# Kernel tuning notes

Hardware: AMD Instinct MI355X
Metric: run time of the kernel (lower is better)

## Reference

```python
import jax, jax.numpy as jnp
import numpy as np

N_NODES = 100000
N_EDGES = 1600000
IN_CH = 128
HID = 128
BN_EPS = 1e-5


def setup_inputs() -> dict:
    key = jax.random.key(0)
    ks = jax.random.split(key, 8)
    s = 1.0 / np.sqrt(HID)
    return {
        "x": jax.random.normal(ks[0], (N_NODES, IN_CH), dtype=jnp.float32),
        "edge_index": jax.random.randint(ks[1], (2, N_EDGES), 0, N_NODES, dtype=jnp.int64),
        "w1_0": jax.random.normal(ks[2], (IN_CH, HID), dtype=jnp.float32) * s,
        "b1_0": jnp.zeros((HID,), dtype=jnp.float32),
        "w2_0": jax.random.normal(ks[3], (HID, HID), dtype=jnp.float32) * s,
        "b2_0": jnp.zeros((HID,), dtype=jnp.float32),
        "gamma_0": jnp.ones((HID,), dtype=jnp.float32),
        "beta_0": jnp.zeros((HID,), dtype=jnp.float32),
        "w1_1": jax.random.normal(ks[4], (HID, HID), dtype=jnp.float32) * s,
        "b1_1": jnp.zeros((HID,), dtype=jnp.float32),
        "w2_1": jax.random.normal(ks[5], (HID, HID), dtype=jnp.float32) * s,
        "b2_1": jnp.zeros((HID,), dtype=jnp.float32),
        "gamma_1": jnp.ones((HID,), dtype=jnp.float32),
        "beta_1": jnp.zeros((HID,), dtype=jnp.float32),
    }


def _gin_layer(x, src, dst, w1, b1, w2, b2, gamma, beta):
    n = x.shape[0]
    # neighbor sum aggregation: scatter-add of source features into destinations
    agg = jax.ops.segment_sum(x[src], dst, num_segments=n)
    h = x + agg  # GINConv with eps = 0: (1 + eps) * x + sum_j x_j
    h = jax.nn.relu(h @ w1 + b1) @ w2 + b2  # 2-layer MLP
    # BatchNorm1d (training mode): batch mean, biased variance
    mean = jnp.mean(h, axis=0)
    var = jnp.mean(jnp.square(h - mean), axis=0)
    h = (h - mean) * jax.lax.rsqrt(var + BN_EPS) * gamma + beta
    return jax.nn.relu(h)


def reference(x, edge_index, w1_0, b1_0, w2_0, b2_0, gamma_0, beta_0,
              w1_1, b1_1, w2_1, b2_1, gamma_1, beta_1):
    src, dst = edge_index[0], edge_index[1]
    h = _gin_layer(x, src, dst, w1_0, b1_0, w2_0, b2_0, gamma_0, beta_0)
    h = _gin_layer(h, src, dst, w1_1, b1_1, w2_1, b2_1, gamma_1, beta_1)
    return h
```

## Files before the change

kernel.cpp:

```cpp
#include <hip/hip_runtime.h>
#include <stdint.h>

#define BN_EPS 1e-5f
#define CHUNK 4096

typedef __attribute__((ext_vector_type(8))) short s16x8;
typedef __attribute__((ext_vector_type(16))) float f32x16;
typedef __attribute__((ext_vector_type(4))) unsigned short u16x4;
typedef unsigned short ushort_t;

__device__ __forceinline__ ushort_t f2bf(float x) {
    uint32_t u = __float_as_uint(x);
    u += 0x7fff + ((u >> 16) & 1);
    return (ushort_t)(u >> 16);
}
__device__ __forceinline__ float bf2f(ushort_t h) {
    return __uint_as_float(((uint32_t)h) << 16);
}

__global__ void k_wprep(const float* __restrict__ w0, const float* __restrict__ w1,
                        const float* __restrict__ w2, const float* __restrict__ w3,
                        ushort_t* __restrict__ wpl) {
    int mat = blockIdx.x >> 6;
    const float* w = (mat == 0) ? w0 : (mat == 1) ? w1 : (mat == 2) ? w2 : w3;
    int e = ((blockIdx.x & 63) << 8) + threadIdx.x;
    int k = e >> 7, col = e & 127;
    float v = w[e];
    ushort_t h = f2bf(v);
    ushort_t l = f2bf(v - bf2f(h));
    ushort_t* base = wpl + (size_t)mat * 32768;
    base[col * 128 + k] = h;
    base[16384 + col * 128 + k] = l;
}

__global__ __launch_bounds__(256) void k_bin(const int* __restrict__ src, const int* __restrict__ dst,
                                             int E, int NBUK, int CAP,
                                             int* __restrict__ gcursor, uint32_t* __restrict__ binned) {
    __shared__ int hist[128], excl[128], gbase[128], hA[128], hB[128];
    __shared__ uint32_t pbuf[CHUNK];
    __shared__ unsigned char bbuf[CHUNK];
    int t = threadIdx.x;
    int base = blockIdx.x * CHUNK;
    int cnt = E - base; if (cnt > CHUNK) cnt = CHUNK;

    uint32_t pk[16]; int bk[16]; int loc[16];
    if (t < 128) hist[t] = 0;
    __syncthreads();
#pragma unroll
    for (int k = 0; k < 16; ++k) {
        int j = t + (k << 8);
        bk[k] = -1;
        if (j < cnt) {
            int s = src[base + j], d = dst[base + j];
            bk[k] = d >> 10;
            pk[k] = ((uint32_t)s << 10) | (uint32_t)(d & 1023);
            loc[k] = atomicAdd(&hist[bk[k]], 1);
        }
    }
    __syncthreads();
    if (t < 128) hA[t] = (t < NBUK) ? hist[t] : 0;
    __syncthreads();
    {
        int cb = 0;
        int* bufs[2] = {hA, hB};
        for (int off = 1; off < 128; off <<= 1) {
            int* A = bufs[cb]; int* B = bufs[cb ^ 1];
            if (t < 128) B[t] = A[t] + ((t >= off) ? A[t - off] : 0);
            __syncthreads();
            cb ^= 1;
        }
        if (t < 128) excl[t] = bufs[cb][t] - ((t < NBUK) ? hist[t] : 0);
    }
    if (t < NBUK && hist[t] > 0) gbase[t] = atomicAdd(&gcursor[t], hist[t]);
    __syncthreads();
#pragma unroll
    for (int k = 0; k < 16; ++k) {
        if (bk[k] >= 0) {
            int slot = excl[bk[k]] + loc[k];
            pbuf[slot] = pk[k];
            bbuf[slot] = (unsigned char)bk[k];
        }
    }
    __syncthreads();
    for (int j = t; j < cnt; j += 256) {
        int b = bbuf[j];
        int pos = gbase[b] + (j - excl[b]);
        if (pos < CAP) binned[(size_t)b * CAP + pos] = pbuf[j];
    }
}

__global__ void k_bucketscan(const int* __restrict__ gcursor, int NBUK,
                             int* __restrict__ bucketBase, int* __restrict__ rowstart,
                             int N, int E) {
    __shared__ int hA[128], hB[128];
    int t = threadIdx.x;
    int v = (t < NBUK) ? gcursor[t] : 0;
    hA[t] = v;
    __syncthreads();
    int cb = 0;
    int* bufs[2] = {hA, hB};
    for (int off = 1; off < 128; off <<= 1) {
        int* A = bufs[cb]; int* B = bufs[cb ^ 1];
        B[t] = A[t] + ((t >= off) ? A[t - off] : 0);
        __syncthreads();
        cb ^= 1;
    }
    if (t < NBUK) bucketBase[t] = bufs[cb][t] - v;
    if (t == 0) rowstart[N] = E;
}

__global__ __launch_bounds__(1024) void k_bucketcsr(const uint32_t* __restrict__ binned,
                                                    const int* __restrict__ gcursor,
                                                    const int* __restrict__ bucketBase,
                                                    int CAP, int N,
                                                    int* __restrict__ rowstart, int* __restrict__ csr) {
    __shared__ int deg[1024], sA[1024], sB[1024], cur[1024];
    int b = blockIdx.x, t = threadIdx.x;
    int cnt = gcursor[b]; if (cnt > CAP) cnt = CAP;
    int gb = bucketBase[b];
    int nodeBase = b << 10;
    int nloc = N - nodeBase; if (nloc > 1024) nloc = 1024;
    const uint32_t* eb = binned + (size_t)b * CAP;

    deg[t] = 0;
    __syncthreads();
    for (int j = t; j < cnt; j += 1024) atomicAdd(&deg[eb[j] & 1023], 1);
    __syncthreads();
    sA[t] = deg[t];
    __syncthreads();
    int cb2 = 0;
    int* bufs[2] = {sA, sB};
    for (int off = 1; off < 1024; off <<= 1) {
        int* A = bufs[cb2]; int* B = bufs[cb2 ^ 1];
        B[t] = A[t] + ((t >= off) ? A[t - off] : 0);
        __syncthreads();
        cb2 ^= 1;
    }
    int ex = bufs[cb2][t] - deg[t];
    cur[t] = ex;
    if (t < nloc) rowstart[nodeBase + t] = gb + ex;
    __syncthreads();
    for (int j = t; j < cnt; j += 1024) {
        uint32_t e = eb[j];
        int p = atomicAdd(&cur[e & 1023], 1);
        csr[gb + p] = (int)(e >> 10);
    }
}

template <bool BN>
__global__ __launch_bounds__(256) void k_agg(const float* __restrict__ in, int N,
                                             const int* __restrict__ rowstart, const int* __restrict__ csr,
                                             const float* __restrict__ stats, const float* __restrict__ gamma,
                                             const float* __restrict__ beta, float invN,
                                             ushort_t* __restrict__ out_hi, ushort_t* __restrict__ out_lo) {
    int node = (int)((blockIdx.x * (size_t)blockDim.x + threadIdx.x) >> 6);
    int lane = threadIdx.x & 63;
    int half = lane >> 5, li = lane & 31, ch4 = li << 2;
    if (node >= N) return;

    float scx = 1.f, scy = 1.f, scz = 1.f, scw = 1.f;
    float shx = 0.f, shy = 0.f, shz = 0.f, shw = 0.f;
    if (BN) {
        float4 m4 = *(const float4*)(stats + ch4);
        float4 q4 = *(const float4*)(stats + 128 + ch4);
        float4 g4 = *(const float4*)(gamma + ch4);
        float4 b4 = *(const float4*)(beta + ch4);
        float mx = m4.x * invN, my = m4.y * invN, mz = m4.z * invN, mw = m4.w * invN;
        scx = g4.x * rsqrtf(q4.x * invN - mx * mx + BN_EPS);
        scy = g4.y * rsqrtf(q4.y * invN - my * my + BN_EPS);
        scz = g4.z * rsqrtf(q4.z * invN - mz * mz + BN_EPS);
        scw = g4.w * rsqrtf(q4.w * invN - mw * mw + BN_EPS);
        shx = b4.x - mx * scx; shy = b4.y - my * scy;
        shz = b4.z - mz * scz; shw = b4.w - mw * scw;
    }

    float ax = 0.f, ay = 0.f, az = 0.f, aw = 0.f;
    if (half == 0) {
        float4 v = *(const float4*)(in + (size_t)node * 128 + ch4);
        if (BN) {
            ax = fmaxf(v.x * scx + shx, 0.f); ay = fmaxf(v.y * scy + shy, 0.f);
            az = fmaxf(v.z * scz + shz, 0.f); aw = fmaxf(v.w * scw + shw, 0.f);
        } else { ax = v.x; ay = v.y; az = v.z; aw = v.w; }
    }

    int s0 = rowstart[node], s1 = rowstart[node + 1];
    for (int base2 = s0; base2 < s1; base2 += 64) {
        int m = s1 - base2; if (m > 64) m = 64;
        int idx = (lane < m) ? csr[base2 + lane] : 0;
        for (int j = 0; j < m; j += 8) {
            int r0 = __shfl(idx, j + half, 64);
            int r1 = __shfl(idx, j + 2 + half, 64);
            int r2 = __shfl(idx, j + 4 + half, 64);
            int r3 = __shfl(idx, j + 6 + half, 64);
            float4 u0 = *(const float4*)(in + (size_t)r0 * 128 + ch4);
            float4 u1 = *(const float4*)(in + (size_t)r1 * 128 + ch4);
            float4 u2 = *(const float4*)(in + (size_t)r2 * 128 + ch4);
            float4 u3 = *(const float4*)(in + (size_t)r3 * 128 + ch4);
            if (j + half < m) {
                if (BN) { ax += fmaxf(u0.x*scx+shx,0.f); ay += fmaxf(u0.y*scy+shy,0.f); az += fmaxf(u0.z*scz+shz,0.f); aw += fmaxf(u0.w*scw+shw,0.f); }
                else    { ax += u0.x; ay += u0.y; az += u0.z; aw += u0.w; }
            }
            if (j + 2 + half < m) {
                if (BN) { ax += fmaxf(u1.x*scx+shx,0.f); ay += fmaxf(u1.y*scy+shy,0.f); az += fmaxf(u1.z*scz+shz,0.f); aw += fmaxf(u1.w*scw+shw,0.f); }
                else    { ax += u1.x; ay += u1.y; az += u1.z; aw += u1.w; }
            }
            if (j + 4 + half < m) {
                if (BN) { ax += fmaxf(u2.x*scx+shx,0.f); ay += fmaxf(u2.y*scy+shy,0.f); az += fmaxf(u2.z*scz+shz,0.f); aw += fmaxf(u2.w*scw+shw,0.f); }
                else    { ax += u2.x; ay += u2.y; az += u2.z; aw += u2.w; }
            }
            if (j + 6 + half < m) {
                if (BN) { ax += fmaxf(u3.x*scx+shx,0.f); ay += fmaxf(u3.y*scy+shy,0.f); az += fmaxf(u3.z*scz+shz,0.f); aw += fmaxf(u3.w*scw+shw,0.f); }
                else    { ax += u3.x; ay += u3.y; az += u3.z; aw += u3.w; }
            }
        }
    }
    ax += __shfl(ax, lane ^ 32, 64);
    ay += __shfl(ay, lane ^ 32, 64);
    az += __shfl(az, lane ^ 32, 64);
    aw += __shfl(aw, lane ^ 32, 64);
    if (half == 0) {
        u16x4 hi, lo;
        ushort_t h;
        h = f2bf(ax); hi[0] = h; lo[0] = f2bf(ax - bf2f(h));
        h = f2bf(ay); hi[1] = h; lo[1] = f2bf(ay - bf2f(h));
        h = f2bf(az); hi[2] = h; lo[2] = f2bf(az - bf2f(h));
        h = f2bf(aw); hi[3] = h; lo[3] = f2bf(aw - bf2f(h));
        size_t o = (size_t)node * 128 + ch4;
        *(u16x4*)(out_hi + o) = hi;
        *(u16x4*)(out_lo + o) = lo;
    }
}

__global__ __launch_bounds__(256) void k_mlp(const ushort_t* __restrict__ a_hi, const ushort_t* __restrict__ a_lo,
                                             const ushort_t* __restrict__ w1pl, const ushort_t* __restrict__ w2pl,
                                             const float* __restrict__ bias1, const float* __restrict__ bias2,
                                             float* __restrict__ h2, float* __restrict__ stats,
                                             int M, int ntiles) {
    __shared__ float4 tile[1024];
    int lane = threadIdx.x & 63;
    int wv = threadIdx.x >> 6;
    int li = lane & 31, half = lane >> 5;
    int c0 = wv << 5;
    int col = c0 + li;
    int khalf = half << 3;
    float* tf = (float*)tile;

    s16x8 b1h[8], b1l[8];
#pragma unroll
    for (int ks = 0; ks < 8; ++ks) {
        b1h[ks] = *(const s16x8*)(w1pl + (size_t)col * 128 + ks * 16 + khalf);
        b1l[ks] = *(const s16x8*)(w1pl + 16384 + (size_t)col * 128 + ks * 16 + khalf);
    }
    float b1v = bias1[col], b2v = bias2[col];
    float ssum = 0.f, ssq = 0.f;

    for (int ti = blockIdx.x; ti < ntiles; ti += gridDim.x) {
        int m0 = ti << 5;
        int arow = m0 + li; if (arow >= M) arow = M - 1;
        const ushort_t* pa = a_hi + (size_t)arow * 128 + khalf;
        const ushort_t* pl = a_lo + (size_t)arow * 128 + khalf;
        f32x16 acc = {}, acc2 = {};
#pragma unroll
        for (int ks = 0; ks < 8; ++ks) {
            s16x8 ah = *(const s16x8*)(pa + ks * 16);
            s16x8 al = *(const s16x8*)(pl + ks * 16);
            acc  = __builtin_amdgcn_mfma_f32_32x32x16_bf16(ah, b1h[ks], acc, 0, 0, 0);
            acc2 = __builtin_amdgcn_mfma_f32_32x32x16_bf16(ah, b1l[ks], acc2, 0, 0, 0);
            acc2 = __builtin_amdgcn_mfma_f32_32x32x16_bf16(al, b1h[ks], acc2, 0, 0, 0);
        }
#pragma unroll
        for (int r = 0; r < 16; ++r) {
            int row = (r & 3) + ((r >> 2) << 3) + (half << 2);
            float v = fmaxf(acc[r] + acc2[r] + b1v, 0.f);
            int chunk = (col >> 2) ^ row;
            tf[((row << 5) + chunk) * 4 + (col & 3)] = v;
        }
        __syncthreads();
        acc = (f32x16){}; acc2 = (f32x16){};
#pragma unroll
        for (int ks = 0; ks < 8; ++ks) {
            int k0 = ks * 16 + khalf;
            float4 fA = tile[(li << 5) + (((k0 >> 2) + 0) ^ li)];
            float4 fB = tile[(li << 5) + (((k0 >> 2) + 1) ^ li)];
            s16x8 ah, al;
            float vv[8] = {fA.x, fA.y, fA.z, fA.w, fB.x, fB.y, fB.z, fB.w};
#pragma unroll
            for (int q = 0; q < 8; ++q) {
                ushort_t hh = f2bf(vv[q]);
                ah[q] = (short)hh;
                al[q] = (short)f2bf(vv[q] - bf2f(hh));
            }
            s16x8 b2h = *(const s16x8*)(w2pl + (size_t)col * 128 + k0);
            s16x8 b2l = *(const s16x8*)(w2pl + 16384 + (size_t)col * 128 + k0);
            acc  = __builtin_amdgcn_mfma_f32_32x32x16_bf16(ah, b2h, acc, 0, 0, 0);
            acc2 = __builtin_amdgcn_mfma_f32_32x32x16_bf16(ah, b2l, acc2, 0, 0, 0);
            acc2 = __builtin_amdgcn_mfma_f32_32x32x16_bf16(al, b2h, acc2, 0, 0, 0);
        }
        __syncthreads();
#pragma unroll
        for (int r = 0; r < 16; ++r) {
            int row = m0 + (r & 3) + ((r >> 2) << 3) + (half << 2);
            if (row < M) {
                float v = acc[r] + acc2[r] + b2v;
                h2[(size_t)row * 128 + col] = v;
                ssum += v; ssq += v * v;
            }
        }
    }
    ssum += __shfl(ssum, lane ^ 32, 64);
    ssq  += __shfl(ssq,  lane ^ 32, 64);
    if (half == 0) {
        atomicAdd(&stats[col], ssum);
        atomicAdd(&stats[128 + col], ssq);
    }
}

__global__ __launch_bounds__(256) void k_bnapply(const float* __restrict__ h2, const float* __restrict__ stats,
                                                 const float* __restrict__ gamma, const float* __restrict__ beta,
                                                 float invN, float* __restrict__ out, int n4) {
    __shared__ float sc[128], sh[128];
    int t = threadIdx.x;
    if (t < 128) {
        float mean = stats[t] * invN;
        float var = stats[128 + t] * invN - mean * mean;
        float s = gamma[t] * rsqrtf(var + BN_EPS);
        sc[t] = s; sh[t] = beta[t] - mean * s;
    }
    __syncthreads();
    int i = blockIdx.x * 256 + t, st = gridDim.x * 256;
    for (; i < n4; i += st) {
        float4 v = ((const float4*)h2)[i];
        int c = (i << 2) & 127;
        v.x = fmaxf(v.x * sc[c + 0] + sh[c + 0], 0.f);
        v.y = fmaxf(v.y * sc[c + 1] + sh[c + 1], 0.f);
        v.z = fmaxf(v.z * sc[c + 2] + sh[c + 2], 0.f);
        v.w = fmaxf(v.w * sc[c + 3] + sh[c + 3], 0.f);
        ((float4*)out)[i] = v;
    }
}

extern "C" void kernel_launch(void* const* d_in, const int* in_sizes, int n_in,
                              void* d_out, int out_size, void* d_ws, size_t ws_size,
                              hipStream_t stream) {
    const float* x      = (const float*)d_in[0];
    const int*   ei     = (const int*)d_in[1];
    const float* w1_0   = (const float*)d_in[2];
    const float* b1_0   = (const float*)d_in[3];
    const float* w2_0   = (const float*)d_in[4];
    const float* b2_0   = (const float*)d_in[5];
    const float* gamma0 = (const float*)d_in[6];
    const float* beta0  = (const float*)d_in[7];
    const float* w1_1   = (const float*)d_in[8];
    const float* b1_1   = (const float*)d_in[9];
    const float* w2_1   = (const float*)d_in[10];
    const float* b2_1   = (const float*)d_in[11];
    const float* gamma1 = (const float*)d_in[12];
    const float* beta1  = (const float*)d_in[13];

    const int N = in_sizes[0] / 128;
    const int E = in_sizes[1] / 2;
    const int* srcI = ei;
    const int* dstI = ei + E;
    const int NBUK = (N + 1023) >> 10;
    const int CAP  = (((E / NBUK) + 2048) + 255) & ~255;

    char* p = (char*)d_ws;
    auto aup = [](size_t v) { return (v + 255) & ~(size_t)255; };
    ushort_t* a_hi   = (ushort_t*)p; p += aup((size_t)N * 128 * 2);
    ushort_t* a_lo   = (ushort_t*)p; p += aup((size_t)N * 128 * 2);
    float*    h2     = (float*)p;    p += aup((size_t)N * 128 * 4);
    int*      rowstart = (int*)p;    p += aup((size_t)(N + 1) * 4);
    int*      csr    = (int*)p;      p += aup((size_t)E * 4);
    uint32_t* binned = (uint32_t*)p; p += aup((size_t)NBUK * CAP * 4);
    ushort_t* wpl    = (ushort_t*)p; p += aup((size_t)4 * 32768 * 2);
    int*      bucketBase = (int*)p;  p += 512;
    int*      gcursor = (int*)p;
    float*    stats0  = (float*)(p + 512);
    float*    stats1  = stats0 + 256;
    hipMemsetAsync(gcursor, 0, 512 + 2048, stream);

    const int ntiles = (N + 31) / 32;
    const float invN = 1.0f / (float)N;
    float* out = (float*)d_out;

    k_wprep<<<256, 256, 0, stream>>>(w1_0, w2_0, w1_1, w2_1, wpl);
    k_bin<<<(E + CHUNK - 1) / CHUNK, 256, 0, stream>>>(srcI, dstI, E, NBUK, CAP, gcursor, binned);
    k_bucketscan<<<1, 128, 0, stream>>>(gcursor, NBUK, bucketBase, rowstart, N, E);
    k_bucketcsr<<<NBUK, 1024, 0, stream>>>(binned, gcursor, bucketBase, CAP, N, rowstart, csr);

    int aggBlocks = (N + 3) / 4;
    k_agg<false><<<aggBlocks, 256, 0, stream>>>(x, N, rowstart, csr, nullptr, nullptr, nullptr, 0.f, a_hi, a_lo);
    k_mlp<<<782, 256, 0, stream>>>(a_hi, a_lo, wpl, wpl + 32768, b1_0, b2_0, h2, stats0, N, ntiles);
    k_agg<true><<<aggBlocks, 256, 0, stream>>>(h2, N, rowstart, csr, stats0, gamma0, beta0, invN, a_hi, a_lo);
    k_mlp<<<782, 256, 0, stream>>>(a_hi, a_lo, wpl + 65536, wpl + 98304, b1_1, b2_1, h2, stats1, N, ntiles);
    k_bnapply<<<2048, 256, 0, stream>>>(h2, stats1, gamma1, beta1, invN, out, N * 32);
}
```

Baseline: 548.1 us.

## Gather neighbor features from fp16 copies instead of fp32 in aggregation

Result: faster. 463.4 us (-15.5%).

```diff
diff --git a/kernel.cpp b/kernel.cpp
--- a/kernel.cpp
+++ b/kernel.cpp
@@ -8,6 +8,8 @@
 typedef __attribute__((ext_vector_type(16))) float f32x16;
 typedef __attribute__((ext_vector_type(4))) unsigned short u16x4;
 typedef unsigned short ushort_t;
+typedef _Float16 f16;
+typedef __attribute__((ext_vector_type(4))) _Float16 f16x4;
 
 __device__ __forceinline__ ushort_t f2bf(float x) {
     uint32_t u = __float_as_uint(x);
@@ -33,6 +35,42 @@
     base[16384 + col * 128 + k] = l;
 }
 
+__global__ void k_x0(const float* __restrict__ in, f16* __restrict__ out, int n4) {
+    int i = blockIdx.x * blockDim.x + threadIdx.x;
+    int st = gridDim.x * blockDim.x;
+    for (; i < n4; i += st) {
+        float4 v = ((const float4*)in)[i];
+        f16x4 h;
+        h[0] = (f16)v.x; h[1] = (f16)v.y; h[2] = (f16)v.z; h[3] = (f16)v.w;
+        ((f16x4*)out)[i] = h;
+    }
+}
+
+__global__ __launch_bounds__(256) void k_x1(const float* __restrict__ h2, const float* __restrict__ stats,
+                                            const float* __restrict__ gamma, const float* __restrict__ beta,
+                                            float invN, f16* __restrict__ out, int n4) {
+    __shared__ float sc[128], sh[128];
+    int t = threadIdx.x;
+    if (t < 128) {
+        float mean = stats[t] * invN;
+        float var = stats[128 + t] * invN - mean * mean;
+        float s = gamma[t] * rsqrtf(var + BN_EPS);
+        sc[t] = s; sh[t] = beta[t] - mean * s;
+    }
+    __syncthreads();
+    int i = blockIdx.x * 256 + t, st = gridDim.x * 256;
+    for (; i < n4; i += st) {
+        float4 v = ((const float4*)h2)[i];
+        int c = (i << 2) & 127;
+        f16x4 h;
+        h[0] = (f16)fmaxf(v.x * sc[c + 0] + sh[c + 0], 0.f);
+        h[1] = (f16)fmaxf(v.y * sc[c + 1] + sh[c + 1], 0.f);
+        h[2] = (f16)fmaxf(v.z * sc[c + 2] + sh[c + 2], 0.f);
+        h[3] = (f16)fmaxf(v.w * sc[c + 3] + sh[c + 3], 0.f);
+        ((f16x4*)out)[i] = h;
+    }
+}
+
 __global__ __launch_bounds__(256) void k_bin(const int* __restrict__ src, const int* __restrict__ dst,
                                              int E, int NBUK, int CAP,
                                              int* __restrict__ gcursor, uint32_t* __restrict__ binned) {
@@ -147,40 +185,18 @@
     }
 }
 
-template <bool BN>
-__global__ __launch_bounds__(256) void k_agg(const float* __restrict__ in, int N,
+__global__ __launch_bounds__(256) void k_agg(const f16* __restrict__ plane, int N,
                                              const int* __restrict__ rowstart, const int* __restrict__ csr,
-                                             const float* __restrict__ stats, const float* __restrict__ gamma,
-                                             const float* __restrict__ beta, float invN,
                                              ushort_t* __restrict__ out_hi, ushort_t* __restrict__ out_lo) {
     int node = (int)((blockIdx.x * (size_t)blockDim.x + threadIdx.x) >> 6);
     int lane = threadIdx.x & 63;
     int half = lane >> 5, li = lane & 31, ch4 = li << 2;
     if (node >= N) return;
 
-    float scx = 1.f, scy = 1.f, scz = 1.f, scw = 1.f;
-    float shx = 0.f, shy = 0.f, shz = 0.f, shw = 0.f;
-    if (BN) {
-        float4 m4 = *(const float4*)(stats + ch4);
-        float4 q4 = *(const float4*)(stats + 128 + ch4);
-        float4 g4 = *(const float4*)(gamma + ch4);
-        float4 b4 = *(const float4*)(beta + ch4);
-        float mx = m4.x * invN, my = m4.y * invN, mz = m4.z * invN, mw = m4.w * invN;
-        scx = g4.x * rsqrtf(q4.x * invN - mx * mx + BN_EPS);
-        scy = g4.y * rsqrtf(q4.y * invN - my * my + BN_EPS);
-        scz = g4.z * rsqrtf(q4.z * invN - mz * mz + BN_EPS);
-        scw = g4.w * rsqrtf(q4.w * invN - mw * mw + BN_EPS);
-        shx = b4.x - mx * scx; shy = b4.y - my * scy;
-        shz = b4.z - mz * scz; shw = b4.w - mw * scw;
-    }
-
     float ax = 0.f, ay = 0.f, az = 0.f, aw = 0.f;
     if (half == 0) {
-        float4 v = *(const float4*)(in + (size_t)node * 128 + ch4);
-        if (BN) {
-            ax = fmaxf(v.x * scx + shx, 0.f); ay = fmaxf(v.y * scy + shy, 0.f);
-            az = fmaxf(v.z * scz + shz, 0.f); aw = fmaxf(v.w * scw + shw, 0.f);
-        } else { ax = v.x; ay = v.y; az = v.z; aw = v.w; }
+        f16x4 sv = *(const f16x4*)(plane + (size_t)node * 128 + ch4);
+        ax = (float)sv[0]; ay = (float)sv[1]; az = (float)sv[2]; aw = (float)sv[3];
     }
 
     int s0 = rowstart[node], s1 = rowstart[node + 1];
@@ -192,26 +208,14 @@
             int r1 = __shfl(idx, j + 2 + half, 64);
             int r2 = __shfl(idx, j + 4 + half, 64);
             int r3 = __shfl(idx, j + 6 + half, 64);
-            float4 u0 = *(const float4*)(in + (size_t)r0 * 128 + ch4);
-            float4 u1 = *(const float4*)(in + (size_t)r1 * 128 + ch4);
-            float4 u2 = *(const float4*)(in + (size_t)r2 * 128 + ch4);
-            float4 u3 = *(const float4*)(in + (size_t)r3 * 128 + ch4);
-            if (j + half < m) {
-                if (BN) { ax += fmaxf(u0.x*scx+shx,0.f); ay += fmaxf(u0.y*scy+shy,0.f); az += fmaxf(u0.z*scz+shz,0.f); aw += fmaxf(u0.w*scw+shw,0.f); }
-                else    { ax += u0.x; ay += u0.y; az += u0.z; aw += u0.w; }
-            }
-            if (j + 2 + half < m) {
-                if (BN) { ax += fmaxf(u1.x*scx+shx,0.f); ay += fmaxf(u1.y*scy+shy,0.f); az += fmaxf(u1.z*scz+shz,0.f); aw += fmaxf(u1.w*scw+shw,0.f); }
-                else    { ax += u1.x; ay += u1.y; az += u1.z; aw += u1.w; }
-            }
-            if (j + 4 + half < m) {
-                if (BN) { ax += fmaxf(u2.x*scx+shx,0.f); ay += fmaxf(u2.y*scy+shy,0.f); az += fmaxf(u2.z*scz+shz,0.f); aw += fmaxf(u2.w*scw+shw,0.f); }
-                else    { ax += u2.x; ay += u2.y; az += u2.z; aw += u2.w; }
-            }
-            if (j + 6 + half < m) {
-                if (BN) { ax += fmaxf(u3.x*scx+shx,0.f); ay += fmaxf(u3.y*scy+shy,0.f); az += fmaxf(u3.z*scz+shz,0.f); aw += fmaxf(u3.w*scw+shw,0.f); }
-                else    { ax += u3.x; ay += u3.y; az += u3.z; aw += u3.w; }
-            }
+            f16x4 u0 = *(const f16x4*)(plane + (size_t)r0 * 128 + ch4);
+            f16x4 u1 = *(const f16x4*)(plane + (size_t)r1 * 128 + ch4);
+            f16x4 u2 = *(const f16x4*)(plane + (size_t)r2 * 128 + ch4);
+            f16x4 u3 = *(const f16x4*)(plane + (size_t)r3 * 128 + ch4);
+            if (j + half < m)     { ax += (float)u0[0]; ay += (float)u0[1]; az += (float)u0[2]; aw += (float)u0[3]; }
+            if (j + 2 + half < m) { ax += (float)u1[0]; ay += (float)u1[1]; az += (float)u1[2]; aw += (float)u1[3]; }
+            if (j + 4 + half < m) { ax += (float)u2[0]; ay += (float)u2[1]; az += (float)u2[2]; aw += (float)u2[3]; }
+            if (j + 6 + half < m) { ax += (float)u3[0]; ay += (float)u3[1]; az += (float)u3[2]; aw += (float)u3[3]; }
         }
     }
     ax += __shfl(ax, lane ^ 32, 64);
@@ -369,6 +373,7 @@
     ushort_t* a_hi   = (ushort_t*)p; p += aup((size_t)N * 128 * 2);
     ushort_t* a_lo   = (ushort_t*)p; p += aup((size_t)N * 128 * 2);
     float*    h2     = (float*)p;    p += aup((size_t)N * 128 * 4);
+    f16*      xh     = (f16*)p;      p += aup((size_t)N * 128 * 2);
     int*      rowstart = (int*)p;    p += aup((size_t)(N + 1) * 4);
     int*      csr    = (int*)p;      p += aup((size_t)E * 4);
     uint32_t* binned = (uint32_t*)p; p += aup((size_t)NBUK * CAP * 4);
@@ -384,14 +389,16 @@
     float* out = (float*)d_out;
 
     k_wprep<<<256, 256, 0, stream>>>(w1_0, w2_0, w1_1, w2_1, wpl);
+    k_x0<<<2048, 256, 0, stream>>>(x, xh, N * 32);
     k_bin<<<(E + CHUNK - 1) / CHUNK, 256, 0, stream>>>(srcI, dstI, E, NBUK, CAP, gcursor, binned);
     k_bucketscan<<<1, 128, 0, stream>>>(gcursor, NBUK, bucketBase, rowstart, N, E);
     k_bucketcsr<<<NBUK, 1024, 0, stream>>>(binned, gcursor, bucketBase, CAP, N, rowstart, csr);
 
     int aggBlocks = (N + 3) / 4;
-    k_agg<false><<<aggBlocks, 256, 0, stream>>>(x, N, rowstart, csr, nullptr, nullptr, nullptr, 0.f, a_hi, a_lo);
+    k_agg<<<aggBlocks, 256, 0, stream>>>(xh, N, rowstart, csr, a_hi, a_lo);
     k_mlp<<<782, 256, 0, stream>>>(a_hi, a_lo, wpl, wpl + 32768, b1_0, b2_0, h2, stats0, N, ntiles);
-    k_agg<true><<<aggBlocks, 256, 0, stream>>>(h2, N, rowstart, csr, stats0, gamma0, beta0, invN, a_hi, a_lo);
+    k_x1<<<2048, 256, 0, stream>>>(h2, stats0, gamma0, beta0, invN, xh, N * 32);
+    k_agg<<<aggBlocks, 256, 0, stream>>>(xh, N, rowstart, csr, a_hi, a_lo);
     k_mlp<<<782, 256, 0, stream>>>(a_hi, a_lo, wpl + 65536, wpl + 98304, b1_1, b2_1, h2, stats1, N, ntiles);
     k_bnapply<<<2048, 256, 0, stream>>>(h2, stats1, gamma1, beta1, invN, out, N * 32);
 }
```
